# Optimization experiments

Hardware: AMD Instinct MI355X
Metric: run time of the kernel (lower is better)

## Reference

```python
import jax, jax.numpy as jnp
import numpy as np

N, E, NODE_IN, EDGE_IN, D, T, OUT = 10000, 80000, 30, 3, 128, 10, 3


def _add_mlp(inp, w, name, din, dout, ln, stack=()):
    inp[name + '_W0'] = w(stack + (din, D))
    inp[name + '_b0'] = jnp.zeros(stack + (D,), jnp.float32)
    inp[name + '_W1'] = w(stack + (D, D))
    inp[name + '_b1'] = jnp.zeros(stack + (D,), jnp.float32)
    inp[name + '_W2'] = w(stack + (D, dout))
    inp[name + '_b2'] = jnp.zeros(stack + (dout,), jnp.float32)
    if ln:
        inp[name + '_g'] = jnp.ones(stack + (dout,), jnp.float32)
        inp[name + '_be'] = jnp.zeros(stack + (dout,), jnp.float32)


def setup_inputs():
    keys = iter(jax.random.split(jax.random.key(0), 32))

    def w(shape, scale=0.1):
        return jax.random.normal(next(keys), shape, jnp.float32) * scale

    inp = {}
    inp['node_feat'] = jax.random.normal(next(keys), (N, NODE_IN), jnp.float32)
    inp['edge_feat'] = jax.random.normal(next(keys), (E, EDGE_IN), jnp.float32)
    inp['senders'] = jax.random.randint(next(keys), (E,), 0, N)
    inp['receivers'] = jax.random.randint(next(keys), (E,), 0, N)
    _add_mlp(inp, w, 'encn', NODE_IN, D, True)
    _add_mlp(inp, w, 'ence', EDGE_IN, D, True)
    _add_mlp(inp, w, 'msg', 3 * D, D, True, (T,))
    _add_mlp(inp, w, 'upd', 2 * D, D, True, (T,))
    _add_mlp(inp, w, 'dec', D, OUT, False)
    return inp


def _mlp3(x, W0, b0, W1, b1, W2, b2):
    # mlp(latent_dim, depth=2, out): two relu hidden layers then linear out
    h = jax.nn.relu(x @ W0 + b0)
    h = jax.nn.relu(h @ W1 + b1)
    return h @ W2 + b2


def _ln(x, g, b, eps=1e-3):
    # keras LayerNormalization (default epsilon=1e-3)
    m = jnp.mean(x, axis=-1, keepdims=True)
    v = jnp.mean(jnp.square(x - m), axis=-1, keepdims=True)
    return g * (x - m) * jax.lax.rsqrt(v + eps) + b


def reference(node_feat, edge_feat, senders, receivers,
              encn_W0, encn_b0, encn_W1, encn_b1, encn_W2, encn_b2, encn_g, encn_be,
              ence_W0, ence_b0, ence_W1, ence_b1, ence_W2, ence_b2, ence_g, ence_be,
              msg_W0, msg_b0, msg_W1, msg_b1, msg_W2, msg_b2, msg_g, msg_be,
              upd_W0, upd_b0, upd_W1, upd_b1, upd_W2, upd_b2, upd_g, upd_be,
              dec_W0, dec_b0, dec_W1, dec_b1, dec_W2, dec_b2):
    n = node_feat.shape[0]
    # encoder: MLP + LayerNorm embeddings of node / edge features
    h = _ln(_mlp3(node_feat, encn_W0, encn_b0, encn_W1, encn_b1, encn_W2, encn_b2), encn_g, encn_be)
    e = _ln(_mlp3(edge_feat, ence_W0, ence_b0, ence_W1, ence_b1, ence_W2, ence_b2), ence_g, ence_be)
    # processor: num_message_passes rounds of gather -> edge MLP -> segment-sum -> node MLP + residual
    for t in range(msg_W0.shape[0]):
        msg_in = jnp.concatenate([h[receivers], h[senders], e], axis=-1)  # [E, 3D]
        m = _ln(_mlp3(msg_in, msg_W0[t], msg_b0[t], msg_W1[t], msg_b1[t], msg_W2[t], msg_b2[t]),
                msg_g[t], msg_be[t])  # [E, D]
        pooled = jax.ops.segment_sum(m, receivers, num_segments=n)  # [N, D]
        upd_in = jnp.concatenate([h, pooled], axis=-1)  # [N, 2D]
        h = h + _ln(_mlp3(upd_in, upd_W0[t], upd_b0[t], upd_W1[t], upd_b1[t], upd_W2[t], upd_b2[t]),
                    upd_g[t], upd_be[t])  # ResidualNextState
    # decoder head (no layer norm)
    return _mlp3(h, dec_W0, dec_b0, dec_W1, dec_b1, dec_W2, dec_b2)
```

## Files before the change

### kernel.cpp

```cpp
#include <hip/hip_runtime.h>

#define NN 10000
#define EE 80000
#define TT 10

typedef unsigned short u16;
typedef unsigned int u32;
using f32x4  = __attribute__((ext_vector_type(4))) float;
using bf16x8 = __attribute__((ext_vector_type(8))) short;

__device__ __forceinline__ u16 f2bf(float f) {
  union { float f; u32 u; } v; v.f = f;
  return (u16)((v.u + 0x7fffu + ((v.u >> 16) & 1u)) >> 16);
}
__device__ __forceinline__ u32 pk2(float lo, float hi) {
  return (u32)f2bf(lo) | ((u32)f2bf(hi) << 16);
}
__device__ __forceinline__ float bflo(u32 v) { union { u32 u; float f; } x; x.u = v << 16; return x.f; }
__device__ __forceinline__ float bfhi(u32 v) { union { u32 u; float f; } x; x.u = v & 0xffff0000u; return x.f; }

__device__ __forceinline__ int xcd_swz(int orig, int nwg) {
  int q = nwg >> 3, r = nwg & 7;
  int xcd = orig & 7, idx = orig >> 3;
  return (xcd < r ? xcd * (q + 1) : r * (q + 1) + (xcd - r) * q) + idx;
}


__global__ __launch_bounds__(256) void hist_k(const int* __restrict__ rcv, int* __restrict__ cnt) {
  int e = blockIdx.x * 256 + threadIdx.x;
  if (e < EE) atomicAdd(&cnt[rcv[e]], 1);
}

__global__ __launch_bounds__(1024) void scan_k(const int* __restrict__ cnt,
                                               int* __restrict__ offs, int* __restrict__ curs) {
  __shared__ int ps[1024];
  const int t = threadIdx.x;
  int loc[10], s = 0;
  #pragma unroll
  for (int j = 0; j < 10; ++j) {
    int idx = t * 10 + j;
    int v = (idx < NN) ? cnt[idx] : 0;
    loc[j] = s; s += v;
  }
  ps[t] = s;
  __syncthreads();
  for (int off = 1; off < 1024; off <<= 1) {
    int v = (t >= off) ? ps[t - off] : 0;
    __syncthreads();
    ps[t] += v;
    __syncthreads();
  }
  int pre = (t == 0) ? 0 : ps[t - 1];
  #pragma unroll
  for (int j = 0; j < 10; ++j) {
    int idx = t * 10 + j;
    if (idx < NN) { int o = pre + loc[j]; offs[idx] = o; curs[idx] = o; }
  }
  if (t == 1023) offs[NN] = ps[1023];
}

__global__ __launch_bounds__(256) void scatter_k(const int* __restrict__ rcv,
                                                 const int* __restrict__ snd,
                                                 int* __restrict__ curs,
                                                 int* __restrict__ sortpos,
                                                 int* __restrict__ rcv_s,
                                                 int* __restrict__ snd_s) {
  int e = blockIdx.x * 256 + threadIdx.x;
  if (e < EE) {
    int r = rcv[e];
    int p = atomicAdd(&curs[r], 1);
    sortpos[e] = p;
    rcv_s[p] = r;
    snd_s[p] = snd[e];
  }
}

#define NJOBS 16
struct WAll {
  const float* src[NJOBS];
  u16*         dst[NJOBS];
  int          K[NJOBS];
  int          kpad[NJOBS];
  long         tstr[NJOBS];
  int          start[NJOBS + 1];
};

__global__ __launch_bounds__(256) void wtrans_all_k(WAll ja) {
  __shared__ float tile[32][33];
  const int b = blockIdx.x;
  int j = 0;
  while (j < NJOBS - 1 && b >= ja.start[j + 1]) ++j;
  const int rem = b - ja.start[j];
  if (ja.K[j] > 0) {
    const int K = ja.K[j];
    const int tiles_per_t = (K / 32) * 4;
    const int t  = rem / tiles_per_t;
    const int r2 = rem - t * tiles_per_t;
    const int kt = r2 >> 2, nt = r2 & 3;
    const float* s = ja.src[j] + (size_t)t * ja.tstr[j];
    u16* d = ja.dst[j] + (size_t)t * 128 * K;
    const int r = threadIdx.x >> 5, c = threadIdx.x & 31;
    for (int rr = r; rr < 32; rr += 8)
      tile[rr][c] = s[(size_t)(kt * 32 + rr) * 128 + nt * 32 + c];
    __syncthreads();
    for (int rr = r; rr < 32; rr += 8)
      d[(size_t)(nt * 32 + rr) * K + kt * 32 + c] = f2bf(tile[c][rr]);
  } else {
    const int Kr = ja.kpad[j];
    const int ch = threadIdx.x;
    if (ch < 128)
      for (int k = 0; k < 64; ++k)
        ja.dst[j][ch * 64 + k] = (k < Kr) ? f2bf(ja.src[j][(size_t)k * 128 + ch]) : (u16)0;
  }
}

template<int MODE, int KT0, int BM, int WAVES, int MINW>
__global__ __launch_bounds__(WAVES * 64, MINW) void mlp3_mfma_k(
    const u16* __restrict__ h_bf, const u16* __restrict__ e_bf,
    const float* __restrict__ h32, const float* __restrict__ pooled,
    const float* __restrict__ feat,
    const int* __restrict__ snd, const int* __restrict__ rcv,
    const int* __restrict__ sortpos,
    const float* __restrict__ Ur_in, const float* __restrict__ Us_in,
    const u16* __restrict__ Wt0, const float* __restrict__ b0,
    const u16* __restrict__ Wt1, const float* __restrict__ b1,
    const u16* __restrict__ Wt2, const float* __restrict__ b2,
    const float* __restrict__ g,  const float* __restrict__ be,
    const u16* __restrict__ Wtr, const u16* __restrict__ Wts,
    const float* __restrict__ b0n,
    float* __restrict__ h_out, u16* __restrict__ hbf_out,
    float* __restrict__ Ur_out, float* __restrict__ Us_out,
    const u16* __restrict__ dWt0, const float* __restrict__ db0,
    const u16* __restrict__ dWt1, const float* __restrict__ db1,
    const float* __restrict__ dW2, const float* __restrict__ db2,
    float* __restrict__ dec_out) {
  constexpr int K0   = KT0 * 64;
  constexpr int THREADS = WAVES * 64;
  constexpr int WN   = WAVES / 2;
  constexpr int RH   = BM / WN;
  constexpr int NET  = RH / 16;
  constexpr int RPW  = BM / WAVES;
  constexpr int NI   = RPW / 8;
  constexpr int CPW  = 128 / WAVES;
  constexpr int NIW  = CPW / 8;

  __shared__ u16 XS[2][BM * 64];
  __shared__ u16 WS[2][128 * 64];
  __shared__ float part_s[2][BM], part_q[2][BM];

  const int tid = threadIdx.x;
  const int lane = tid & 63;
  const int wq = tid >> 6;
  const int wm = wq / WN, wn = wq % WN;
  const int l15 = lane & 15, lq = lane >> 4;
  const int row0 = xcd_swz(blockIdx.x, gridDim.x) * BM;
  const int lr = lane >> 3;
  const int cj = lane & 7;
  const int ch0 = wm * 64 + lq * 4;

  f32x4 us[4][(MODE == 0) ? NET : 1];
  if constexpr (MODE == 0) {
    #pragma unroll
    for (int et = 0; et < NET; ++et) {
      int ns = snd[row0 + wn * RH + et * 16 + l15];
      #pragma unroll
      for (int ct = 0; ct < 4; ++ct)
        us[ct][et] = *(const f32x4*)(Us_in + (size_t)ns * 128 + ch0 + ct * 16);
    }
  }

  auto load_x = [&](int kt, uint4 v[NI]) {
    #pragma unroll
    for (int i = 0; i < NI; ++i) {
      int q = wq * RPW + i * 8 + lr;
      if constexpr (MODE == 0) {
        v[i] = *(const uint4*)(e_bf + (size_t)(row0 + q) * 128 + kt * 64 + cj * 8);
      } else if constexpr (MODE == 1) {
        int gn = row0 + q;
        if (gn < NN) {
          if (kt < 2) {
            v[i] = *(const uint4*)(h_bf + (size_t)gn * 128 + kt * 64 + cj * 8);
          } else {
            const float* p = pooled + (size_t)gn * 128 + (kt - 2) * 64 + cj * 8;
            float4 a = *(const float4*)p;
            float4 b = *(const float4*)(p + 4);
            v[i].x = pk2(a.x, a.y); v[i].y = pk2(a.z, a.w);
            v[i].z = pk2(b.x, b.y); v[i].w = pk2(b.z, b.w);
          }
        } else v[i] = make_uint4(0, 0, 0, 0);
      } else if constexpr (MODE == 2) {
        int gn = row0 + q;
        float x[8];
        #pragma unroll
        for (int j = 0; j < 8; ++j) {
          int k = cj * 8 + j;
          x[j] = (gn < NN && k < 30) ? feat[(size_t)gn * 30 + k] : 0.f;
        }
        v[i].x = pk2(x[0], x[1]); v[i].y = pk2(x[2], x[3]);
        v[i].z = pk2(x[4], x[5]); v[i].w = pk2(x[6], x[7]);
      } else {
        int ge = row0 + q;
        float x[8];
        #pragma unroll
        for (int j = 0; j < 8; ++j) {
          int k = cj * 8 + j;
          x[j] = (k < 3) ? feat[(size_t)ge * 3 + k] : 0.f;
        }
        v[i].x = pk2(x[0], x[1]); v[i].y = pk2(x[2], x[3]);
        v[i].z = pk2(x[4], x[5]); v[i].w = pk2(x[6], x[7]);
      }
    }
  };
  auto load_w = [&](const u16* Wt, int kstr, int kt, uint4 v[NIW]) {
    #pragma unroll
    for (int i = 0; i < NIW; ++i) {
      int ch = wq * CPW + i * 8 + lr;
      v[i] = *(const uint4*)(Wt + (size_t)ch * kstr + kt * 64 + cj * 8);
    }
  };
  auto stage_x = [&](int buf, const uint4 v[NI]) {
    #pragma unroll
    for (int i = 0; i < NI; ++i) {
      int q = wq * RPW + i * 8 + lr;
      int c = cj ^ (lr & 7);
      *(uint4*)&XS[buf][q * 64 + c * 8] = v[i];
    }
  };
  auto stage_w = [&](int buf, const uint4 v[NIW]) {
    #pragma unroll
    for (int i = 0; i < NIW; ++i) {
      int q = wq * CPW + i * 8 + lr;
      int c = cj ^ (lr & 7);
      *(uint4*)&WS[buf][q * 64 + c * 8] = v[i];
    }
  };

  f32x4 acc[4][NET];
  auto init_acc = [&](const float* b) {
    #pragma unroll
    for (int ct = 0; ct < 4; ++ct) {
      f32x4 bv = {0.f, 0.f, 0.f, 0.f};
      if (b) bv = *(const f32x4*)(b + ch0 + ct * 16);
      #pragma unroll
      for (int et = 0; et < NET; ++et) acc[ct][et] = bv;
    }
  };
  auto compute_tile = [&](const u16* xbuf, const u16* wbuf) {
    #pragma unroll
    for (int k0 = 0; k0 < 2; ++k0) {
      bf16x8 wf[4], xf[NET];
      #pragma unroll
      for (int ct = 0; ct < 4; ++ct) {
        int ch = wm * 64 + ct * 16 + l15;
        wf[ct] = *(const bf16x8*)&wbuf[ch * 64 + (((k0 * 4 + lq) ^ (l15 & 7)) * 8)];
      }
      #pragma unroll
      for (int et = 0; et < NET; ++et) {
        int ed = wn * RH + et * 16 + l15;
        xf[et] = *(const bf16x8*)&xbuf[ed * 64 + (((k0 * 4 + lq) ^ (l15 & 7)) * 8)];
      }
      #pragma unroll
      for (int ct = 0; ct < 4; ++ct)
        #pragma unroll
        for (int et = 0; et < NET; ++et)
          acc[ct][et] = __builtin_amdgcn_mfma_f32_16x16x32_bf16(wf[ct], xf[et], acc[ct][et], 0, 0, 0);
    }
  };
  auto layer128 = [&](const u16* Wt, const float* b, uint4 vwl[NIW]) {
    init_acc(b);
    load_w(Wt, 128, 0, vwl); stage_w(0, vwl);
    __syncthreads();
    for (int kt = 0; kt < 2; ++kt) {
      if (kt < 1) load_w(Wt, 128, 1, vwl);
      compute_tile(XS[kt], WS[kt]);
      if (kt < 1) stage_w(1, vwl);
      __syncthreads();
    }
  };
  auto store_h = [&](bool relu) {
    #pragma unroll
    for (int ct = 0; ct < 4; ++ct)
      #pragma unroll
      for (int et = 0; et < NET; ++et) {
        float v0 = acc[ct][et][0], v1 = acc[ct][et][1], v2 = acc[ct][et][2], v3 = acc[ct][et][3];
        if (relu) { v0 = fmaxf(v0, 0.f); v1 = fmaxf(v1, 0.f); v2 = fmaxf(v2, 0.f); v3 = fmaxf(v3, 0.f); }
        ushort4 o = {f2bf(v0), f2bf(v1), f2bf(v2), f2bf(v3)};
        int ed = wn * RH + et * 16 + l15;
        int c3 = ct * 2 + (lq >> 1);
        int cs = c3 ^ (l15 & 7);
        *(ushort4*)&XS[wm][ed * 64 + cs * 8 + (lq & 1) * 4] = o;
      }
  };

  uint4 vx[NI], vw[NIW];

  if constexpr (MODE == 0) init_acc(nullptr); else init_acc(b0);
  load_x(0, vx); load_w(Wt0, K0, 0, vw);
  stage_x(0, vx); stage_w(0, vw);
  __syncthreads();
  for (int kt = 0; kt < KT0; ++kt) {
    int cur = kt & 1, nxt = cur ^ 1;
    if (kt < KT0 - 1) { load_x(kt + 1, vx); load_w(Wt0, K0, kt + 1, vw); }
    compute_tile(XS[cur], WS[cur]);
    if (kt < KT0 - 1) { stage_x(nxt, vx); stage_w(nxt, vw); }
    __syncthreads();
  }
  if constexpr (MODE == 1) {
    float* pz = (float*)pooled;
    #pragma unroll
    for (int i = 0; i < NI; ++i) {
      int gn = row0 + wq * RPW + i * 8 + lr;
      if (gn < NN) {
        float4 z = {0.f, 0.f, 0.f, 0.f};
        #pragma unroll
        for (int kt2 = 0; kt2 < 2; ++kt2) {
          *(float4*)(pz + (size_t)gn * 128 + kt2 * 64 + cj * 8) = z;
          *(float4*)(pz + (size_t)gn * 128 + kt2 * 64 + cj * 8 + 4) = z;
        }
      }
    }
  }
  if constexpr (MODE == 0) {
    #pragma unroll
    for (int et = 0; et < NET; ++et) {
      int nr = rcv[row0 + wn * RH + et * 16 + l15];
      #pragma unroll
      for (int ct = 0; ct < 4; ++ct) {
        f32x4 vr = *(const f32x4*)(Ur_in + (size_t)nr * 128 + ch0 + ct * 16);
        acc[ct][et] += vr + us[ct][et];
      }
    }
  }
  store_h(true);
  __syncthreads();

  layer128(Wt1, b1, vw);
  store_h(true);
  __syncthreads();
  layer128(Wt2, b2, vw);

  float ss[NET], qs[NET];
  #pragma unroll
  for (int et = 0; et < NET; ++et) {
    float s = 0.f, q = 0.f;
    #pragma unroll
    for (int ct = 0; ct < 4; ++ct)
      #pragma unroll
      for (int i = 0; i < 4; ++i) { float v = acc[ct][et][i]; s += v; q += v * v; }
    s += __shfl_xor(s, 16, 64); s += __shfl_xor(s, 32, 64);
    q += __shfl_xor(q, 16, 64); q += __shfl_xor(q, 32, 64);
    ss[et] = s; qs[et] = q;
  }
  if (lane < 16) {
    #pragma unroll
    for (int et = 0; et < NET; ++et) {
      part_s[wm][wn * RH + et * 16 + lane] = ss[et];
      part_q[wm][wn * RH + et * 16 + lane] = qs[et];
    }
  }
  __syncthreads();
  float mean[NET], inv[NET];
  #pragma unroll
  for (int et = 0; et < NET; ++et) {
    int ed = wn * RH + et * 16 + l15;
    float S = part_s[0][ed] + part_s[1][ed];
    float Q = part_q[0][ed] + part_q[1][ed];
    float m = S * (1.f / 128.f);
    float var = Q * (1.f / 128.f) - m * m;
    mean[et] = m; inv[et] = rsqrtf(var + 1e-3f);
  }
  #pragma unroll
  for (int ct = 0; ct < 4; ++ct) {
    f32x4 g4 = *(const f32x4*)(g  + ch0 + ct * 16);
    f32x4 b4 = *(const f32x4*)(be + ch0 + ct * 16);
    #pragma unroll
    for (int et = 0; et < NET; ++et)
      #pragma unroll
      for (int i = 0; i < 4; ++i)
        acc[ct][et][i] = g4[i] * (acc[ct][et][i] - mean[et]) * inv[et] + b4[i];
  }

  if constexpr (MODE == 0) {
    store_h(false);
    __syncthreads();
    const int* offs = sortpos;
    const int nf = rcv[row0];
    const int nl = rcv[row0 + BM - 1];
    const int cg = tid & 15;
    const int buf = cg >> 3, c3 = cg & 7;
    constexpr int NG = THREADS / 16;
    for (int n = nf + (tid >> 4); n <= nl; n += NG) {
      int s0 = offs[n], s1 = offs[n + 1];
      int a = max(s0, row0) - row0, b = min(s1, row0 + BM) - row0;
      if (a >= b) continue;
      float a8[8] = {0.f, 0.f, 0.f, 0.f, 0.f, 0.f, 0.f, 0.f};
      for (int r = a; r < b; ++r) {
        uint4 v = *(const uint4*)&XS[buf][r * 64 + ((c3 ^ (r & 7)) * 8)];
        a8[0] += bflo(v.x); a8[1] += bfhi(v.x);
        a8[2] += bflo(v.y); a8[3] += bfhi(v.y);
        a8[4] += bflo(v.z); a8[5] += bfhi(v.z);
        a8[6] += bflo(v.w); a8[7] += bfhi(v.w);
      }
      float* pp = h_out + (size_t)n * 128 + cg * 8;
      if (s0 >= row0 && s1 <= row0 + BM) {
        float4 o0 = {a8[0], a8[1], a8[2], a8[3]};
        float4 o1 = {a8[4], a8[5], a8[6], a8[7]};
        *(float4*)pp = o0;
        *(float4*)(pp + 4) = o1;
      } else {
        #pragma unroll
        for (int j = 0; j < 8; ++j) atomicAdd(pp + j, a8[j]);
      }
    }
  } else if constexpr (MODE == 3) {
    int gp[NET];
    #pragma unroll
    for (int et = 0; et < NET; ++et)
      gp[et] = sortpos[row0 + wn * RH + et * 16 + l15];
    #pragma unroll
    for (int ct = 0; ct < 4; ++ct)
      #pragma unroll
      for (int et = 0; et < NET; ++et) {
        f32x4 v = acc[ct][et];
        ushort4 o = {f2bf(v[0]), f2bf(v[1]), f2bf(v[2]), f2bf(v[3])};
        *(ushort4*)(hbf_out + (size_t)gp[et] * 128 + ch0 + ct * 16) = o;
      }
  } else {
    #pragma unroll
    for (int ct = 0; ct < 4; ++ct)
      #pragma unroll
      for (int et = 0; et < NET; ++et) {
        int gr = row0 + wn * RH + et * 16 + l15;
        if (gr < NN) {
          if constexpr (MODE == 1)
            acc[ct][et] += *(const f32x4*)(h32 + (size_t)gr * 128 + ch0 + ct * 16);
          f32x4 v = acc[ct][et];
          ushort4 o = {f2bf(v[0]), f2bf(v[1]), f2bf(v[2]), f2bf(v[3])};
          *(f32x4*)(h_out + (size_t)gr * 128 + ch0 + ct * 16) = v;
          *(ushort4*)(hbf_out + (size_t)gr * 128 + ch0 + ct * 16) = o;
        }
      }
    if (Wtr) {
      store_h(false);
      __syncthreads();
      layer128(Wtr, b0n, vw);
      #pragma unroll
      for (int ct = 0; ct < 4; ++ct)
        #pragma unroll
        for (int et = 0; et < NET; ++et) {
          int gr = row0 + wn * RH + et * 16 + l15;
          if (gr < NN)
            *(f32x4*)(Ur_out + (size_t)gr * 128 + ch0 + ct * 16) = acc[ct][et];
        }
      layer128(Wts, nullptr, vw);
      #pragma unroll
      for (int ct = 0; ct < 4; ++ct)
        #pragma unroll
        for (int et = 0; et < NET; ++et) {
          int gr = row0 + wn * RH + et * 16 + l15;
          if (gr < NN)
            *(f32x4*)(Us_out + (size_t)gr * 128 + ch0 + ct * 16) = acc[ct][et];
        }
    } else if (MODE == 1 && dWt0) {
      store_h(false);
      __syncthreads();
      layer128(dWt0, db0, vw);
      store_h(true);
      __syncthreads();
      layer128(dWt1, db1, vw);
      store_h(true);
      __syncthreads();
      if (tid < BM * 3) {
        int r = tid / 3, o = tid - (tid / 3) * 3;
        int gn = row0 + r;
        float a = db2[o];
        #pragma unroll
        for (int c = 0; c < 16; ++c) {
          int buf = c >> 3, c3 = c & 7, cs = c3 ^ (r & 7);
          uint4 v = *(const uint4*)&XS[buf][r * 64 + cs * 8];
          int k = c * 8;
          a = fmaf(bflo(v.x), dW2[(k + 0) * 3 + o], a);
          a = fmaf(bfhi(v.x), dW2[(k + 1) * 3 + o], a);
          a = fmaf(bflo(v.y), dW2[(k + 2) * 3 + o], a);
          a = fmaf(bfhi(v.y), dW2[(k + 3) * 3 + o], a);
          a = fmaf(bflo(v.z), dW2[(k + 4) * 3 + o], a);
          a = fmaf(bfhi(v.z), dW2[(k + 5) * 3 + o], a);
          a = fmaf(bflo(v.w), dW2[(k + 6) * 3 + o], a);
          a = fmaf(bfhi(v.w), dW2[(k + 7) * 3 + o], a);
        }
        if (gn < NN) dec_out[(size_t)gn * 3 + o] = a;
      }
    }
  }
}

extern "C" void kernel_launch(void* const* d_in, const int* in_sizes, int n_in,
                              void* d_out, int out_size, void* d_ws, size_t ws_size,
                              hipStream_t stream) {
  int i = 0;
  const float* node_feat = (const float*)d_in[i++];
  const float* edge_feat = (const float*)d_in[i++];
  const int*   senders   = (const int*)d_in[i++];
  const int*   receivers = (const int*)d_in[i++];
  const float *encn_W0 = (const float*)d_in[i++], *encn_b0 = (const float*)d_in[i++],
              *encn_W1 = (const float*)d_in[i++], *encn_b1 = (const float*)d_in[i++],
              *encn_W2 = (const float*)d_in[i++], *encn_b2 = (const float*)d_in[i++],
              *encn_g  = (const float*)d_in[i++], *encn_be = (const float*)d_in[i++];
  const float *ence_W0 = (const float*)d_in[i++], *ence_b0 = (const float*)d_in[i++],
              *ence_W1 = (const float*)d_in[i++], *ence_b1 = (const float*)d_in[i++],
              *ence_W2 = (const float*)d_in[i++], *ence_b2 = (const float*)d_in[i++],
              *ence_g  = (const float*)d_in[i++], *ence_be = (const float*)d_in[i++];
  const float *msg_W0 = (const float*)d_in[i++], *msg_b0 = (const float*)d_in[i++],
              *msg_W1 = (const float*)d_in[i++], *msg_b1 = (const float*)d_in[i++],
              *msg_W2 = (const float*)d_in[i++], *msg_b2 = (const float*)d_in[i++],
              *msg_g  = (const float*)d_in[i++], *msg_be = (const float*)d_in[i++];
  const float *upd_W0 = (const float*)d_in[i++], *upd_b0 = (const float*)d_in[i++],
              *upd_W1 = (const float*)d_in[i++], *upd_b1 = (const float*)d_in[i++],
              *upd_W2 = (const float*)d_in[i++], *upd_b2 = (const float*)d_in[i++],
              *upd_g  = (const float*)d_in[i++], *upd_be = (const float*)d_in[i++];
  const float *dec_W0 = (const float*)d_in[i++], *dec_b0 = (const float*)d_in[i++],
              *dec_W1 = (const float*)d_in[i++], *dec_b1 = (const float*)d_in[i++],
              *dec_W2 = (const float*)d_in[i++], *dec_b2 = (const float*)d_in[i++];

  char* w = (char*)d_ws;
  float* h      = (float*)w;            w += (size_t)NN * 128 * 4;
  float* pooled = (float*)w;            w += (size_t)NN * 128 * 4;
  float* Ur     = (float*)w;            w += (size_t)NN * 128 * 4;
  float* Us     = (float*)w;            w += (size_t)NN * 128 * 4;
  u16*   h_bf   = (u16*)w;              w += (size_t)NN * 128 * 2;
  u16*   e_bf   = (u16*)w;              w += (size_t)EE * 128 * 2;
  u16*   mWt0e  = (u16*)w;              w += (size_t)10 * 128 * 128 * 2;
  u16*   mWt1   = (u16*)w;              w += (size_t)10 * 128 * 128 * 2;
  u16*   mWt2   = (u16*)w;              w += (size_t)10 * 128 * 128 * 2;
  u16*   pWtr   = (u16*)w;              w += (size_t)10 * 128 * 128 * 2;
  u16*   pWts   = (u16*)w;              w += (size_t)10 * 128 * 128 * 2;
  u16*   uWt0   = (u16*)w;              w += (size_t)10 * 128 * 256 * 2;
  u16*   uWt1   = (u16*)w;              w += (size_t)10 * 128 * 128 * 2;
  u16*   uWt2   = (u16*)w;              w += (size_t)10 * 128 * 128 * 2;
  u16*   nWt0   = (u16*)w;              w += (size_t)128 * 64 * 2;
  u16*   nWt1   = (u16*)w;              w += (size_t)128 * 128 * 2;
  u16*   nWt2   = (u16*)w;              w += (size_t)128 * 128 * 2;
  u16*   eWt0   = (u16*)w;              w += (size_t)128 * 64 * 2;
  u16*   eWt1   = (u16*)w;              w += (size_t)128 * 128 * 2;
  u16*   eWt2   = (u16*)w;              w += (size_t)128 * 128 * 2;
  u16*   dWt0   = (u16*)w;              w += (size_t)128 * 128 * 2;
  u16*   dWt1   = (u16*)w;              w += (size_t)128 * 128 * 2;
  int*   cnt    = (int*)w;              w += (size_t)NN * 4;
  int*   offs   = (int*)w;              w += (size_t)(NN + 1) * 4;
  int*   curs   = (int*)w;              w += (size_t)NN * 4;
  int*   sortp  = (int*)w;              w += (size_t)EE * 4;
  int*   rcv_s  = (int*)w;              w += (size_t)EE * 4;
  int*   snd_s  = (int*)w;              w += (size_t)EE * 4;

  const int NB_N64 = (NN + 63) / 64;
  const int NB_N32 = (NN + 31) / 32;
  const int NB_E128 = EE / 128;
  const int NB_E256 = (EE + 255) / 256;

  hipMemsetAsync(cnt, 0, (size_t)NN * 4, stream);
  hipMemsetAsync(pooled, 0, (size_t)NN * 128 * 4, stream);
  hist_k<<<NB_E256, 256, 0, stream>>>(receivers, cnt);
  scan_k<<<1, 1024, 0, stream>>>(cnt, offs, curs);
  scatter_k<<<NB_E256, 256, 0, stream>>>(receivers, senders, curs, sortp, rcv_s, snd_s);

  {
    WAll ja;
    const float* srcs[NJOBS] = {
      msg_W0, msg_W0 + 128 * 128, msg_W0 + 256 * 128, msg_W1, msg_W2,
      upd_W0, upd_W1, upd_W2,
      encn_W1, encn_W2, ence_W1, ence_W2, dec_W0, dec_W1,
      encn_W0, ence_W0 };
    u16* dsts[NJOBS] = {
      pWtr, pWts, mWt0e, mWt1, mWt2,
      uWt0, uWt1, uWt2,
      nWt1, nWt2, eWt1, eWt2, dWt0, dWt1,
      nWt0, eWt0 };
    int  Ks[NJOBS]   = {128,128,128,128,128, 256,128,128, 128,128,128,128,128,128, 0,0};
    int  kps[NJOBS]  = {0,0,0,0,0, 0,0,0, 0,0,0,0,0,0, 30,3};
    long tss[NJOBS]  = {384*128,384*128,384*128,128*128,128*128,
                        256*128,128*128,128*128, 0,0,0,0,0,0, 0,0};
    int  nts[NJOBS]  = {10,10,10,10,10, 10,10,10, 1,1,1,1,1,1, 1,1};
    int acc = 0;
    for (int j = 0; j < NJOBS; ++j) {
      ja.src[j] = srcs[j]; ja.dst[j] = dsts[j];
      ja.K[j] = Ks[j]; ja.kpad[j] = kps[j]; ja.tstr[j] = tss[j];
      ja.start[j] = acc;
      acc += (Ks[j] > 0) ? nts[j] * (Ks[j] / 32) * 4 : 1;
    }
    ja.start[NJOBS] = acc;
    wtrans_all_k<<<acc, 256, 0, stream>>>(ja);
  }

  mlp3_mfma_k<2, 1, 64, 4, 2><<<NB_N64, 256, 0, stream>>>(
      nullptr, nullptr, nullptr, nullptr, node_feat, nullptr, nullptr, nullptr,
      nullptr, nullptr,
      nWt0, encn_b0, nWt1, encn_b1, nWt2, encn_b2, encn_g, encn_be,
      pWtr, pWts, msg_b0,
      h, h_bf, Ur, Us,
      nullptr, nullptr, nullptr, nullptr, nullptr, nullptr, nullptr);
  mlp3_mfma_k<3, 1, 128, 4, 2><<<NB_E128, 256, 0, stream>>>(
      nullptr, nullptr, nullptr, nullptr, edge_feat, nullptr, nullptr, sortp,
      nullptr, nullptr,
      eWt0, ence_b0, eWt1, ence_b1, eWt2, ence_b2, ence_g, ence_be,
      nullptr, nullptr, nullptr,
      nullptr, e_bf, nullptr, nullptr,
      nullptr, nullptr, nullptr, nullptr, nullptr, nullptr, nullptr);

  for (int t = 0; t < TT; ++t) {
    mlp3_mfma_k<0, 2, 128, 8, 4><<<NB_E128, 512, 0, stream>>>(
        nullptr, e_bf, nullptr, nullptr, nullptr, snd_s, rcv_s, offs,
        Ur, Us,
        mWt0e + (size_t)t * 128 * 128, nullptr,
        mWt1  + (size_t)t * 128 * 128, msg_b1 + (size_t)t * 128,
        mWt2  + (size_t)t * 128 * 128, msg_b2 + (size_t)t * 128,
        msg_g + (size_t)t * 128, msg_be + (size_t)t * 128,
        nullptr, nullptr, nullptr,
        pooled, nullptr, nullptr, nullptr,
        nullptr, nullptr, nullptr, nullptr, nullptr, nullptr, nullptr);
    bool last = (t == TT - 1);
    mlp3_mfma_k<1, 4, 32, 4, 4><<<NB_N32, 256, 0, stream>>>(
        h_bf, nullptr, h, pooled, nullptr, nullptr, nullptr, nullptr,
        nullptr, nullptr,
        uWt0 + (size_t)t * 128 * 256, upd_b0 + (size_t)t * 128,
        uWt1 + (size_t)t * 128 * 128, upd_b1 + (size_t)t * 128,
        uWt2 + (size_t)t * 128 * 128, upd_b2 + (size_t)t * 128,
        upd_g + (size_t)t * 128, upd_be + (size_t)t * 128,
        last ? nullptr : (pWtr + (size_t)(t + 1) * 128 * 128),
        last ? nullptr : (pWts + (size_t)(t + 1) * 128 * 128),
        last ? nullptr : (msg_b0 + (size_t)(t + 1) * 128),
        h, h_bf, Ur, Us,
        last ? dWt0 : nullptr, last ? dec_b0 : nullptr,
        last ? dWt1 : nullptr, last ? dec_b1 : nullptr,
        last ? dec_W2 : nullptr, last ? dec_b2 : nullptr,
        last ? (float*)d_out : nullptr);
  }
}
```

Before: 606.4 us.

## Single-buffer weight LDS, add MFMA priority, shrink edge-kernel tile to 64 rows

Replaces the double-buffered weight tile in shared memory with a single buffer, staged between extra barriers, so each block uses less LDS. It wraps the MFMA loop in s_setprio so matrix work is issued ahead of other waves. The per-step message kernel moves from 128-edge blocks of 512 threads to 64-edge blocks of 256 threads, aiming for higher occupancy and more blocks. The trade-off is extra __syncthreads and less overlap between weight loads and compute.

```diff
diff --git a/kernel.cpp b/kernel.cpp
--- a/kernel.cpp
+++ b/kernel.cpp
@@ -145,7 +145,7 @@
   constexpr int NIW  = CPW / 8;
 
   __shared__ u16 XS[2][BM * 64];
-  __shared__ u16 WS[2][128 * 64];
+  __shared__ u16 WS[128 * 64];
   __shared__ float part_s[2][BM], part_q[2][BM];
 
   const int tid = threadIdx.x;
@@ -226,12 +226,12 @@
       *(uint4*)&XS[buf][q * 64 + c * 8] = v[i];
     }
   };
-  auto stage_w = [&](int buf, const uint4 v[NIW]) {
+  auto stage_w = [&](const uint4 v[NIW]) {
     #pragma unroll
     for (int i = 0; i < NIW; ++i) {
       int q = wq * CPW + i * 8 + lr;
       int c = cj ^ (lr & 7);
-      *(uint4*)&WS[buf][q * 64 + c * 8] = v[i];
+      *(uint4*)&WS[q * 64 + c * 8] = v[i];
     }
   };
 
@@ -245,36 +245,38 @@
       for (int et = 0; et < NET; ++et) acc[ct][et] = bv;
     }
   };
-  auto compute_tile = [&](const u16* xbuf, const u16* wbuf) {
+  auto compute_tile = [&](const u16* xbuf) {
     #pragma unroll
     for (int k0 = 0; k0 < 2; ++k0) {
       bf16x8 wf[4], xf[NET];
       #pragma unroll
       for (int ct = 0; ct < 4; ++ct) {
         int ch = wm * 64 + ct * 16 + l15;
-        wf[ct] = *(const bf16x8*)&wbuf[ch * 64 + (((k0 * 4 + lq) ^ (l15 & 7)) * 8)];
+        wf[ct] = *(const bf16x8*)&WS[ch * 64 + (((k0 * 4 + lq) ^ (l15 & 7)) * 8)];
       }
       #pragma unroll
       for (int et = 0; et < NET; ++et) {
         int ed = wn * RH + et * 16 + l15;
         xf[et] = *(const bf16x8*)&xbuf[ed * 64 + (((k0 * 4 + lq) ^ (l15 & 7)) * 8)];
       }
+      __builtin_amdgcn_s_setprio(1);
       #pragma unroll
       for (int ct = 0; ct < 4; ++ct)
         #pragma unroll
         for (int et = 0; et < NET; ++et)
           acc[ct][et] = __builtin_amdgcn_mfma_f32_16x16x32_bf16(wf[ct], xf[et], acc[ct][et], 0, 0, 0);
+      __builtin_amdgcn_s_setprio(0);
     }
   };
   auto layer128 = [&](const u16* Wt, const float* b, uint4 vwl[NIW]) {
     init_acc(b);
-    load_w(Wt, 128, 0, vwl); stage_w(0, vwl);
-    __syncthreads();
+    #pragma unroll 1
     for (int kt = 0; kt < 2; ++kt) {
-      if (kt < 1) load_w(Wt, 128, 1, vwl);
-      compute_tile(XS[kt], WS[kt]);
-      if (kt < 1) stage_w(1, vwl);
+      load_w(Wt, 128, kt, vwl);
       __syncthreads();
+      stage_w(vwl);
+      __syncthreads();
+      compute_tile(XS[kt]);
     }
   };
   auto store_h = [&](bool relu) {
@@ -296,14 +298,18 @@
 
   if constexpr (MODE == 0) init_acc(nullptr); else init_acc(b0);
   load_x(0, vx); load_w(Wt0, K0, 0, vw);
-  stage_x(0, vx); stage_w(0, vw);
+  stage_x(0, vx); stage_w(vw);
   __syncthreads();
+  #pragma unroll 1
   for (int kt = 0; kt < KT0; ++kt) {
-    int cur = kt & 1, nxt = cur ^ 1;
     if (kt < KT0 - 1) { load_x(kt + 1, vx); load_w(Wt0, K0, kt + 1, vw); }
-    compute_tile(XS[cur], WS[cur]);
-    if (kt < KT0 - 1) { stage_x(nxt, vx); stage_w(nxt, vw); }
-    __syncthreads();
+    compute_tile(XS[kt & 1]);
+    if (kt < KT0 - 1) {
+      stage_x((kt + 1) & 1, vx);
+      __syncthreads();
+      stage_w(vw);
+      __syncthreads();
+    }
   }
   if constexpr (MODE == 1) {
     float* pz = (float*)pooled;
@@ -331,12 +337,12 @@
       }
     }
   }
+  __syncthreads();
   store_h(true);
+
+  layer128(Wt1, b1, vw);
   __syncthreads();
-
-  layer128(Wt1, b1, vw);
   store_h(true);
-  __syncthreads();
   layer128(Wt2, b2, vw);
 
   float ss[NET], qs[NET];
@@ -442,7 +448,6 @@
       }
     if (Wtr) {
       store_h(false);
-      __syncthreads();
       layer128(Wtr, b0n, vw);
       #pragma unroll
       for (int ct = 0; ct < 4; ++ct)
@@ -463,11 +468,11 @@
         }
     } else if (MODE == 1 && dWt0) {
       store_h(false);
+      layer128(dWt0, db0, vw);
       __syncthreads();
-      layer128(dWt0, db0, vw);
       store_h(true);
+      layer128(dWt1, db1, vw);
       __syncthreads();
-      layer128(dWt1, db1, vw);
       store_h(true);
       __syncthreads();
       if (tid < BM * 3) {
@@ -554,6 +559,7 @@
 
   const int NB_N64 = (NN + 63) / 64;
   const int NB_N32 = (NN + 31) / 32;
+  const int NB_E64 = EE / 64;
   const int NB_E128 = EE / 128;
   const int NB_E256 = (EE + 255) / 256;
 
@@ -607,7 +613,7 @@
       nullptr, nullptr, nullptr, nullptr, nullptr, nullptr, nullptr);
 
   for (int t = 0; t < TT; ++t) {
-    mlp3_mfma_k<0, 2, 128, 8, 4><<<NB_E128, 512, 0, stream>>>(
+    mlp3_mfma_k<0, 2, 64, 4, 4><<<NB_E64, 256, 0, stream>>>(
         nullptr, e_bf, nullptr, nullptr, nullptr, snd_s, rcv_s, offs,
         Ur, Us,
         mWt0e + (size_t)t * 128 * 128, nullptr,
```

New measurement: 1.053 ms. 73.7% more time.
